# Kernel tuning notes

Hardware: AMD Instinct MI355X
Metric: run time of the kernel (lower is better)

The kernel has to match this reference:

```python
import jax, jax.numpy as jnp
import numpy as np

BN_EPS = 1e-5


def _bn(x, gamma, beta):
    # training-mode BatchNorm1d: biased batch stats over the edge/batch axis
    mean = jnp.mean(x, axis=0, keepdims=True)
    var = jnp.mean((x - mean) ** 2, axis=0, keepdims=True)
    return (x - mean) * jax.lax.rsqrt(var + BN_EPS) * gamma + beta


def setup_inputs() -> dict:
    key = jax.random.key(0)
    ks = jax.random.split(key, 20)
    N, E = 20000, 300000
    in_drug, in_prot, hidden = 256, 512, 256
    h2 = 2 * hidden

    def u(k, shape, fan_in):
        b = 1.0 / np.sqrt(fan_in)
        return jax.random.uniform(k, shape, jnp.float32, -b, b)

    return {
        "x_drug": jax.random.normal(ks[0], (N, in_drug), jnp.float32),
        "x_prot": jax.random.normal(ks[1], (N, in_prot), jnp.float32),
        "edge_index": jax.random.randint(ks[2], (2, E), 0, N, jnp.int64),
        "W_src": u(ks[3], (hidden, in_drug), in_drug),
        "W_dst": u(ks[4], (hidden, in_prot), in_prot),
        "W_gate": u(ks[5], (h2, h2), h2),
        "b_gate": u(ks[6], (h2,), h2),
        "W1": u(ks[7], (hidden, h2), h2),
        "b1": u(ks[8], (hidden,), h2),
        "g1": jnp.ones((hidden,), jnp.float32),
        "be1": jnp.zeros((hidden,), jnp.float32),
        "W2": u(ks[9], (hidden, hidden), hidden),
        "b2": u(ks[10], (hidden,), hidden),
        "g2": jnp.ones((hidden,), jnp.float32),
        "be2": jnp.zeros((hidden,), jnp.float32),
        "W3": u(ks[11], (1, hidden), hidden),
        "b3": u(ks[12], (1,), hidden),
        "W_bil": u(ks[13], (1, hidden, hidden), hidden),
        "b_bil": u(ks[14], (1,), hidden),
    }


def reference(x_drug, x_prot, edge_index, W_src, W_dst, W_gate, b_gate,
              W1, b1, g1, be1, W2, b2, g2, be2, W3, b3, W_bil, b_bil):
    src, dst = edge_index[0], edge_index[1]
    h_src = x_drug[src] @ W_src.T            # [E, H]
    h_dst = x_prot[dst] @ W_dst.T            # [E, H]
    h_cat = jnp.concatenate([h_src, h_dst], axis=1)  # [E, 2H]
    gate = jax.nn.sigmoid(h_cat @ W_gate.T + b_gate)
    h = gate * h_cat
    # MLP (dropout is identity here)
    h1 = jax.nn.relu(_bn(h @ W1.T + b1, g1, be1))
    h2_ = jax.nn.relu(_bn(h1 @ W2.T + b2, g2, be2))
    mlp_score = (h2_ @ W3.T + b3).reshape(-1)
    # Bilinear: out_ek = sum_ij h_src_ei W_kij h_dst_ej + b_k
    bil_score = (jnp.einsum("ei,kij,ej->ek", h_src, W_bil, h_dst) + b_bil).reshape(-1)
    return mlp_score + bil_score
```

## Files before the change

### kernel.cpp

```cpp
#include <hip/hip_runtime.h>
#include <hip/hip_bf16.h>

typedef unsigned short u16;
typedef __attribute__((ext_vector_type(8))) short bf16x8;
typedef __attribute__((ext_vector_type(8))) unsigned short us8;
typedef __attribute__((ext_vector_type(4))) float f32x4;


__device__ __forceinline__ float b2f(u16 u) {
    union { unsigned u32; float f; } x; x.u32 = ((unsigned)u) << 16; return x.f;
}
__device__ __forceinline__ u16 f2b(float f) {
    union { float f; unsigned u; } x; x.f = f;
    unsigned r = x.u + 0x7fffu + ((x.u >> 16) & 1u);
    return (u16)(r >> 16);
}

__global__ __launch_bounds__(256) void zero_kernel(float* p, int n) {
    int i = blockIdx.x * 256 + threadIdx.x;
    if (i < n) p[i] = 0.f;
}

struct CvtSeg { const float* in; u16* out; int n4; };
struct CvtArr { CvtSeg s[6]; int tot4; };
__global__ __launch_bounds__(256) void cvt_fused(CvtArr ca) {
    int i = blockIdx.x * 256 + threadIdx.x;
    if (i >= ca.tot4) return;
    int k = 0, off = i;
#pragma unroll
    for (int q = 0; q < 6; ++q) {
        if (off < ca.s[q].n4) { k = q; break; }
        off -= ca.s[q].n4;
    }
    float4 v = ((const float4*)ca.s[k].in)[off];
    ushort4 o; o.x = f2b(v.x); o.y = f2b(v.y); o.z = f2b(v.z); o.w = f2b(v.w);
    ((ushort4*)ca.s[k].out)[off] = o;
}

struct GDesc {
    const void* A; int lda; int a_f32;
    const u16* W; int ldb;
    u16* C; int ldc;
    int K;
    const float* bias;
};
template <int NY> struct GDescArr { GDesc d[NY]; };

template <int NY>
__global__ __launch_bounds__(256, 2) void mfma_node(GDescArr<NY> da, int M)
{
    const GDesc dd = da.d[blockIdx.y];
    __shared__ u16 As[2][128][40];
    __shared__ u16 Bs[2][256][40];
    const int t = threadIdx.x;
    const int row0 = blockIdx.x * 128;
    const int arow = t >> 1, aks = (t & 1) * 16;
    const int agr = min(row0 + arow, M - 1);
    const int w = t >> 6, lane = t & 63;
    const int wr = w >> 1, wc = w & 1;
    const int lrow = lane & 15, lkg = lane >> 4;
    const int NIT = dd.K >> 5;

    f32x4 acc[4][8] = {};
    us8 ar[2], br[4];
    float4 fr[4];

    auto load_regs = [&](int it) {
        const int k0 = it << 5;
        if (dd.a_f32) {
            const float* ap = (const float*)dd.A + (size_t)agr * dd.lda + k0 + aks;
#pragma unroll
            for (int q = 0; q < 4; ++q) fr[q] = *(const float4*)(ap + q * 4);
        } else {
            const u16* ap = (const u16*)dd.A + (size_t)agr * dd.lda + k0 + aks;
            ar[0] = *(const us8*)ap; ar[1] = *(const us8*)(ap + 8);
        }
        const u16* wp = dd.W + (size_t)t * dd.ldb + k0;
#pragma unroll
        for (int q = 0; q < 4; ++q) br[q] = *(const us8*)(wp + q * 8);
    };
    auto proc_write = [&](int b) {
        if (dd.a_f32) {
#pragma unroll
            for (int q = 0; q < 2; ++q) {
                us8 o;
                const float fq[8] = {fr[q*2].x, fr[q*2].y, fr[q*2].z, fr[q*2].w,
                                     fr[q*2+1].x, fr[q*2+1].y, fr[q*2+1].z, fr[q*2+1].w};
#pragma unroll
                for (int j = 0; j < 8; ++j) o[j] = f2b(fq[j]);
                *(us8*)&As[b][arow][aks + q * 8] = o;
            }
        } else {
            *(us8*)&As[b][arow][aks] = ar[0];
            *(us8*)&As[b][arow][aks + 8] = ar[1];
        }
#pragma unroll
        for (int q = 0; q < 4; ++q) *(us8*)&Bs[b][t][q * 8] = br[q];
    };
    auto do_mfma = [&](int b) {
        bf16x8 af[4];
#pragma unroll
        for (int mi = 0; mi < 4; ++mi)
            af[mi] = *(const bf16x8*)&As[b][wr * 64 + mi * 16 + lrow][lkg * 8];
#pragma unroll
        for (int ni = 0; ni < 8; ++ni) {
            bf16x8 bfr = *(const bf16x8*)&Bs[b][wc * 128 + ni * 16 + lrow][lkg * 8];
#pragma unroll
            for (int mi = 0; mi < 4; ++mi)
                acc[mi][ni] = __builtin_amdgcn_mfma_f32_16x16x32_bf16(
                    af[mi], bfr, acc[mi][ni], 0, 0, 0);
        }
    };

    load_regs(0); proc_write(0); __syncthreads();
    for (int it = 0; it < NIT; ++it) {
        const int cur = it & 1;
        if (it + 1 < NIT) load_regs(it + 1);
        do_mfma(cur);
        if (it + 1 < NIT) proc_write(cur ^ 1);
        __syncthreads();
    }

#pragma unroll
    for (int ni = 0; ni < 8; ++ni) {
        const int gcol = wc * 128 + ni * 16 + lrow;
        const float bv = dd.bias ? dd.bias[gcol] : 0.f;
#pragma unroll
        for (int mi = 0; mi < 4; ++mi) {
            f32x4 v = acc[mi][ni];
#pragma unroll
            for (int j = 0; j < 4; ++j) {
                const int grow = row0 + wr * 64 + mi * 16 + lkg * 4 + j;
                if (grow < M) dd.C[(size_t)grow * dd.ldc + gcol] = f2b(v[j] + bv);
            }
        }
    }
}

#define OP_GATE   1
#define OP_BNRELU 2

template <int AOP>
__global__ __launch_bounds__(256, 3) void mfma_edge(
    const u16* __restrict__ Ain,
    const u16* __restrict__ Wb, int ldb, int K,
    u16* __restrict__ C, int E,
    const int* __restrict__ ei,
    const u16* __restrict__ Gs, const u16* __restrict__ Gd,
    const u16* __restrict__ Hs, const u16* __restrict__ Hd,
    const u16* __restrict__ Bd, const float* __restrict__ b_bil,
    float* __restrict__ bil,
    const float* __restrict__ scaleK, const float* __restrict__ shiftK,
    float* __restrict__ sums)
{
    __shared__ u16 As[2][64][36];
    __shared__ float wsum[2][256];

    const int t = threadIdx.x;
    const int row0 = blockIdx.x * 64;
    const int arow = t >> 2;
    const int aks = (t & 3) * 8;
    const int agr = min(row0 + arow, E - 1);

    int s_ = 0, d_ = 0;
    if constexpr (AOP == OP_GATE) {
        s_ = ei[agr]; d_ = ei[E + agr];
    }

    const int lane = t & 63;
    const int wc = t >> 6;
    const int lrow = lane & 15, lkg = lane >> 4;
    const int NIT = K >> 5;

    f32x4 acc[4][4] = {};
    float bdot = 0.f;
    us8 g1r, g2r, hr, bdr;
    float4 sc0, sc1, sh0, sh1;

    auto load_regs = [&](int it) {
        const int k0 = it << 5;
        const int kg = k0 + aks;
        if constexpr (AOP == OP_GATE) {
            g1r = *(const us8*)(Gs + (size_t)s_ * 512 + kg);
            g2r = *(const us8*)(Gd + (size_t)d_ * 512 + kg);
            hr = (k0 < 256) ? *(const us8*)(Hs + (size_t)s_ * 256 + kg)
                            : *(const us8*)(Hd + (size_t)d_ * 256 + kg - 256);
            if (k0 < 256) bdr = *(const us8*)(Bd + (size_t)d_ * 256 + kg);
        } else {
            g1r = *(const us8*)(Ain + (size_t)agr * 256 + kg);
            sc0 = *(const float4*)(scaleK + kg);
            sc1 = *(const float4*)(scaleK + kg + 4);
            sh0 = *(const float4*)(shiftK + kg);
            sh1 = *(const float4*)(shiftK + kg + 4);
        }
    };
    auto proc_write = [&](int it, int b) {
        const int k0 = it << 5;
        us8 o;
        if constexpr (AOP == OP_GATE) {
#pragma unroll
            for (int j = 0; j < 8; ++j) {
                const float x = b2f(g1r[j]) + b2f(g2r[j]);
                const float g = 1.f / (1.f + __expf(-x));
                o[j] = f2b(g * b2f(hr[j]));
            }
            if (k0 < 256) {
#pragma unroll
                for (int j = 0; j < 8; ++j)
                    bdot = fmaf(b2f(hr[j]), b2f(bdr[j]), bdot);
            }
        } else {
            const float scq[8] = {sc0.x, sc0.y, sc0.z, sc0.w,
                                  sc1.x, sc1.y, sc1.z, sc1.w};
            const float shq[8] = {sh0.x, sh0.y, sh0.z, sh0.w,
                                  sh1.x, sh1.y, sh1.z, sh1.w};
#pragma unroll
            for (int j = 0; j < 8; ++j)
                o[j] = f2b(fmaxf(fmaf(b2f(g1r[j]), scq[j], shq[j]), 0.f));
        }
        *(us8*)&As[b][arow][aks] = o;
    };
    auto do_iter = [&](int it, int b) {
        const int k0 = it << 5;
        bf16x8 bfr[4];
#pragma unroll
        for (int ni = 0; ni < 4; ++ni)
            bfr[ni] = *(const bf16x8*)(Wb +
                (size_t)(wc * 64 + ni * 16 + lrow) * ldb + k0 + lkg * 8);
        bf16x8 af[4];
#pragma unroll
        for (int mi = 0; mi < 4; ++mi)
            af[mi] = *(const bf16x8*)&As[b][mi * 16 + lrow][lkg * 8];
#pragma unroll
        for (int ni = 0; ni < 4; ++ni)
#pragma unroll
            for (int mi = 0; mi < 4; ++mi)
                acc[mi][ni] = __builtin_amdgcn_mfma_f32_16x16x32_bf16(
                    af[mi], bfr[ni], acc[mi][ni], 0, 0, 0);
    };

    load_regs(0); proc_write(0, 0); __syncthreads();
    for (int it = 0; it < NIT; ++it) {
        const int cur = it & 1;
        if (it + 1 < NIT) load_regs(it + 1);
        do_iter(it, cur);
        if (it + 1 < NIT) proc_write(it + 1, cur ^ 1);
        __syncthreads();
    }

    if constexpr (AOP == OP_GATE) {
        bdot += __shfl_xor(bdot, 1, 64);
        bdot += __shfl_xor(bdot, 2, 64);
        if ((t & 3) == 0 && row0 + arow < E)
            bil[row0 + arow] = bdot + b_bil[0];
    }

#pragma unroll
    for (int ni = 0; ni < 4; ++ni) {
        const int gcol = wc * 64 + ni * 16 + lrow;
        float s = 0.f, ss = 0.f;
#pragma unroll
        for (int mi = 0; mi < 4; ++mi) {
            f32x4 v = acc[mi][ni];
#pragma unroll
            for (int j = 0; j < 4; ++j) {
                const int grow = row0 + mi * 16 + lkg * 4 + j;
                const float x = v[j];
                if (grow < E) {
                    C[(size_t)grow * 256 + gcol] = f2b(x);
                    s += x; ss = fmaf(x, x, ss);
                }
            }
        }
        s  += __shfl_xor(s, 16, 64);  s  += __shfl_xor(s, 32, 64);
        ss += __shfl_xor(ss, 16, 64); ss += __shfl_xor(ss, 32, 64);
        if (lkg == 0) { wsum[0][gcol] = s; wsum[1][gcol] = ss; }
    }
    __syncthreads();
    atomicAdd(&sums[t],       wsum[0][t]);
    atomicAdd(&sums[256 + t], wsum[1][t]);
}

__global__ void finalize_kernel(
    const float* __restrict__ sums, const float* __restrict__ g,
    const float* __restrict__ be, int M,
    float* __restrict__ scale, float* __restrict__ shift)
{
    const int c = threadIdx.x;
    const float inv = 1.f / (float)M;
    const float mean = sums[c] * inv;
    const float var  = sums[256 + c] * inv - mean * mean;
    const float sc = g[c] * rsqrtf(var + 1e-5f);
    scale[c] = sc;
    shift[c] = fmaf(-mean, sc, be[c]);
}

__global__ __launch_bounds__(256) void final_kernel(
    const u16* __restrict__ Z2,
    const float* __restrict__ scale2, const float* __restrict__ shift2,
    const float* __restrict__ W3, const float* __restrict__ b3,
    const float* __restrict__ bil,
    float* __restrict__ out, int E)
{
    const int w = threadIdx.x >> 6, lane = threadIdx.x & 63;
    const int e = blockIdx.x * 4 + w;
    if (e >= E) return;
    ushort4 zv = *(const ushort4*)(Z2 + (size_t)e * 256 + lane * 4);
    float4 sc = *(const float4*)(scale2 + lane * 4);
    float4 sh = *(const float4*)(shift2 + lane * 4);
    float4 w3 = *(const float4*)(W3 + lane * 4);
    const u16 zq[4] = {zv.x, zv.y, zv.z, zv.w};
    const float scq[4] = {sc.x, sc.y, sc.z, sc.w};
    const float shq[4] = {sh.x, sh.y, sh.z, sh.w};
    const float wq[4] = {w3.x, w3.y, w3.z, w3.w};
    float acc = 0.f;
#pragma unroll
    for (int i = 0; i < 4; ++i) {
        const float x = fmaxf(fmaf(b2f(zq[i]), scq[i], shq[i]), 0.f);
        acc = fmaf(x, wq[i], acc);
    }
#pragma unroll
    for (int off = 32; off; off >>= 1) acc += __shfl_down(acc, off, 64);
    if (lane == 0) out[e] = acc + b3[0] + bil[e];
}

extern "C" void kernel_launch(void* const* d_in, const int* in_sizes, int n_in,
                              void* d_out, int out_size, void* d_ws, size_t ws_size,
                              hipStream_t stream)
{
    const float* x_drug = (const float*)d_in[0];
    const float* x_prot = (const float*)d_in[1];
    const int*   ei     = (const int*)d_in[2];
    const float* W_src  = (const float*)d_in[3];
    const float* W_dst  = (const float*)d_in[4];
    const float* W_gate = (const float*)d_in[5];
    const float* b_gate = (const float*)d_in[6];
    const float* W1     = (const float*)d_in[7];
    const float* g1     = (const float*)d_in[9];
    const float* be1    = (const float*)d_in[10];
    const float* W2     = (const float*)d_in[11];
    const float* g2     = (const float*)d_in[13];
    const float* be2    = (const float*)d_in[14];
    const float* W3     = (const float*)d_in[15];
    const float* b3     = (const float*)d_in[16];
    const float* W_bil  = (const float*)d_in[17];
    const float* b_bil  = (const float*)d_in[18];
    float* out = (float*)d_out;

    const int N = in_sizes[0] / 256;
    const int E = in_sizes[2] / 2;

    char* wp_ = (char*)d_ws;
    auto alloc = [&](size_t bytes) {
        char* p = wp_; wp_ += (bytes + 255) & ~(size_t)255; return p;
    };
    u16* Wsrcb  = (u16*)alloc(256 * 256 * 2);
    u16* Wdstb  = (u16*)alloc(256 * 512 * 2);
    u16* Wgateb = (u16*)alloc(512 * 512 * 2);
    u16* Wbilb  = (u16*)alloc(256 * 256 * 2);
    u16* W1b    = (u16*)alloc(256 * 512 * 2);
    u16* W2b    = (u16*)alloc(256 * 256 * 2);
    u16* Hs     = (u16*)alloc((size_t)N * 256 * 2);
    u16* Hd     = (u16*)alloc((size_t)N * 256 * 2);
    u16* Gs     = (u16*)alloc((size_t)N * 512 * 2);
    u16* Gd     = (u16*)alloc((size_t)N * 512 * 2);
    u16* Bd     = (u16*)alloc((size_t)N * 256 * 2);
    u16* z      = (u16*)alloc((size_t)E * 256 * 2);
    float* bil  = (float*)alloc((size_t)E * 4);
    float* sums   = (float*)alloc(1024 * 4);
    float* scale1 = (float*)alloc(256 * 4);
    float* shift1 = (float*)alloc(256 * 4);
    float* scale2 = (float*)alloc(256 * 4);
    float* shift2 = (float*)alloc(256 * 4);

    zero_kernel<<<4, 256, 0, stream>>>(sums, 1024);

    CvtArr ca;
    ca.s[0] = {W_src,  Wsrcb,  256 * 256 / 4};
    ca.s[1] = {W_dst,  Wdstb,  256 * 512 / 4};
    ca.s[2] = {W_gate, Wgateb, 512 * 512 / 4};
    ca.s[3] = {W_bil,  Wbilb,  256 * 256 / 4};
    ca.s[4] = {W1,     W1b,    256 * 512 / 4};
    ca.s[5] = {W2,     W2b,    256 * 256 / 4};
    ca.tot4 = 0;
    for (int q = 0; q < 6; ++q) ca.tot4 += ca.s[q].n4;
    cvt_fused<<<(ca.tot4 + 255) / 256, 256, 0, stream>>>(ca);

    const int gxN = (N + 127) / 128;
    const int gxE = (E + 63) / 64;

    GDescArr<2> p1;
    p1.d[0] = {x_drug, 256, 1, Wsrcb, 256, Hs, 256, 256, nullptr};
    p1.d[1] = {x_prot, 512, 1, Wdstb, 512, Hd, 256, 512, nullptr};
    mfma_node<2><<<dim3(gxN, 2), 256, 0, stream>>>(p1, N);

    GDescArr<5> p2;
    p2.d[0] = {Hs, 256, 0, Wgateb,                 512, Gs,       512, 256, b_gate};
    p2.d[1] = {Hs, 256, 0, Wgateb + 256 * 512,     512, Gs + 256, 512, 256, b_gate + 256};
    p2.d[2] = {Hd, 256, 0, Wgateb + 256,           512, Gd,       512, 256, nullptr};
    p2.d[3] = {Hd, 256, 0, Wgateb + 256 * 512 + 256, 512, Gd + 256, 512, 256, nullptr};
    p2.d[4] = {Hd, 256, 0, Wbilb,                  256, Bd,       256, 256, nullptr};
    mfma_node<5><<<dim3(gxN, 5), 256, 0, stream>>>(p2, N);

    mfma_edge<OP_GATE><<<gxE, 256, 0, stream>>>(
        nullptr, W1b, 512, 512, z, E,
        ei, Gs, Gd, Hs, Hd, Bd, b_bil, bil, nullptr, nullptr, sums);
    finalize_kernel<<<1, 256, 0, stream>>>(sums, g1, be1, E, scale1, shift1);

    mfma_edge<OP_BNRELU><<<gxE, 256, 0, stream>>>(
        z, W2b, 256, 256, z, E,
        nullptr, nullptr, nullptr, nullptr, nullptr, nullptr, nullptr, nullptr,
        scale1, shift1, sums + 512);
    finalize_kernel<<<1, 256, 0, stream>>>(sums + 512, g2, be2, E, scale2, shift2);

    final_kernel<<<(E + 3) / 4, 256, 0, stream>>>(
        z, scale2, shift2, W3, b3, bil, out, E);
}
```

Baseline: 630.4 us.

## Stage weight tiles in LDS with 64-wide K slabs in edge MFMA kernel

The edge GEMM kernel now cooperatively loads the 256xK weight slab into shared memory (one row per thread) instead of having each wave read weight fragments straight from global memory, and widens the K step from 32 to 64 per slab. The A-operand preprocessing (gate sigmoid or BN+ReLU) is moved into the register prefetch, with a single LDS buffer plus two barriers per slab. The min-blocks launch bound of 3 is dropped. This cuts redundant global and L2 traffic for weights and halves loop iterations, at the cost of a much larger LDS footprint (about 46 KB), higher register pressure and possibly lower occupancy.

```diff
diff --git a/kernel.cpp b/kernel.cpp
--- a/kernel.cpp
+++ b/kernel.cpp
@@ -141,7 +141,7 @@
 #define OP_BNRELU 2
 
 template <int AOP>
-__global__ __launch_bounds__(256, 3) void mfma_edge(
+__global__ __launch_bounds__(256) void mfma_edge(
     const u16* __restrict__ Ain,
     const u16* __restrict__ Wb, int ldb, int K,
     u16* __restrict__ C, int E,
@@ -153,98 +153,112 @@
     const float* __restrict__ scaleK, const float* __restrict__ shiftK,
     float* __restrict__ sums)
 {
-    __shared__ u16 As[2][64][36];
+    __shared__ u16 As[64][72];
+    __shared__ u16 Bs[256][72];
     __shared__ float wsum[2][256];
 
     const int t = threadIdx.x;
     const int row0 = blockIdx.x * 64;
     const int arow = t >> 2;
-    const int aks = (t & 3) * 8;
+    const int aks  = (t & 3) * 16;
     const int agr = min(row0 + arow, E - 1);
 
     int s_ = 0, d_ = 0;
-    if constexpr (AOP == OP_GATE) {
-        s_ = ei[agr]; d_ = ei[E + agr];
-    }
+    if constexpr (AOP == OP_GATE) { s_ = ei[agr]; d_ = ei[E + agr]; }
 
     const int lane = t & 63;
     const int wc = t >> 6;
     const int lrow = lane & 15, lkg = lane >> 4;
-    const int NIT = K >> 5;
+    const int NKS = K >> 6;
 
     f32x4 acc[4][4] = {};
     float bdot = 0.f;
-    us8 g1r, g2r, hr, bdr;
-    float4 sc0, sc1, sh0, sh1;
-
-    auto load_regs = [&](int it) {
-        const int k0 = it << 5;
-        const int kg = k0 + aks;
+    us8 aw0, aw1, br[8];
+
+    auto loadA = [&](int ks) {
+        const int k = ks * 64 + aks;
         if constexpr (AOP == OP_GATE) {
-            g1r = *(const us8*)(Gs + (size_t)s_ * 512 + kg);
-            g2r = *(const us8*)(Gd + (size_t)d_ * 512 + kg);
-            hr = (k0 < 256) ? *(const us8*)(Hs + (size_t)s_ * 256 + kg)
-                            : *(const us8*)(Hd + (size_t)d_ * 256 + kg - 256);
-            if (k0 < 256) bdr = *(const us8*)(Bd + (size_t)d_ * 256 + kg);
+            us8 gs0 = *(const us8*)(Gs + (size_t)s_ * 512 + k);
+            us8 gs1 = *(const us8*)(Gs + (size_t)s_ * 512 + k + 8);
+            us8 gd0 = *(const us8*)(Gd + (size_t)d_ * 512 + k);
+            us8 gd1 = *(const us8*)(Gd + (size_t)d_ * 512 + k + 8);
+            const u16* hp = (ks < 4) ? (Hs + (size_t)s_ * 256 + k)
+                                     : (Hd + (size_t)d_ * 256 + k - 256);
+            us8 h0 = *(const us8*)hp, h1 = *(const us8*)(hp + 8);
+#pragma unroll
+            for (int j = 0; j < 8; ++j) {
+                const float x0 = b2f(gs0[j]) + b2f(gd0[j]);
+                const float x1 = b2f(gs1[j]) + b2f(gd1[j]);
+                aw0[j] = f2b(b2f(h0[j]) / (1.f + __expf(-x0)));
+                aw1[j] = f2b(b2f(h1[j]) / (1.f + __expf(-x1)));
+            }
+            if (ks < 4) {
+                us8 bd0 = *(const us8*)(Bd + (size_t)d_ * 256 + k);
+                us8 bd1 = *(const us8*)(Bd + (size_t)d_ * 256 + k + 8);
+#pragma unroll
+                for (int j = 0; j < 8; ++j) {
+                    bdot = fmaf(b2f(h0[j]), b2f(bd0[j]), bdot);
+                    bdot = fmaf(b2f(h1[j]), b2f(bd1[j]), bdot);
+                }
+            }
         } else {
-            g1r = *(const us8*)(Ain + (size_t)agr * 256 + kg);
-            sc0 = *(const float4*)(scaleK + kg);
-            sc1 = *(const float4*)(scaleK + kg + 4);
-            sh0 = *(const float4*)(shiftK + kg);
-            sh1 = *(const float4*)(shiftK + kg + 4);
-        }
-    };
-    auto proc_write = [&](int it, int b) {
-        const int k0 = it << 5;
-        us8 o;
-        if constexpr (AOP == OP_GATE) {
+            us8 a0 = *(const us8*)(Ain + (size_t)agr * 256 + k);
+            us8 a1 = *(const us8*)(Ain + (size_t)agr * 256 + k + 8);
+            float4 c0 = *(const float4*)(scaleK + k);
+            float4 c1 = *(const float4*)(scaleK + k + 4);
+            float4 c2 = *(const float4*)(scaleK + k + 8);
+            float4 c3 = *(const float4*)(scaleK + k + 12);
+            float4 h0 = *(const float4*)(shiftK + k);
+            float4 h1 = *(const float4*)(shiftK + k + 4);
+            float4 h2 = *(const float4*)(shiftK + k + 8);
+            float4 h3 = *(const float4*)(shiftK + k + 12);
+            const float scq[16] = {c0.x,c0.y,c0.z,c0.w, c1.x,c1.y,c1.z,c1.w,
+                                   c2.x,c2.y,c2.z,c2.w, c3.x,c3.y,c3.z,c3.w};
+            const float shq[16] = {h0.x,h0.y,h0.z,h0.w, h1.x,h1.y,h1.z,h1.w,
+                                   h2.x,h2.y,h2.z,h2.w, h3.x,h3.y,h3.z,h3.w};
 #pragma unroll
             for (int j = 0; j < 8; ++j) {
-                const float x = b2f(g1r[j]) + b2f(g2r[j]);
-                const float g = 1.f / (1.f + __expf(-x));
-                o[j] = f2b(g * b2f(hr[j]));
-            }
-            if (k0 < 256) {
-#pragma unroll
-                for (int j = 0; j < 8; ++j)
-                    bdot = fmaf(b2f(hr[j]), b2f(bdr[j]), bdot);
-            }
-        } else {
-            const float scq[8] = {sc0.x, sc0.y, sc0.z, sc0.w,
-                                  sc1.x, sc1.y, sc1.z, sc1.w};
-            const float shq[8] = {sh0.x, sh0.y, sh0.z, sh0.w,
-                                  sh1.x, sh1.y, sh1.z, sh1.w};
-#pragma unroll
-            for (int j = 0; j < 8; ++j)
-                o[j] = f2b(fmaxf(fmaf(b2f(g1r[j]), scq[j], shq[j]), 0.f));
-        }
-        *(us8*)&As[b][arow][aks] = o;
-    };
-    auto do_iter = [&](int it, int b) {
-        const int k0 = it << 5;
-        bf16x8 bfr[4];
-#pragma unroll
-        for (int ni = 0; ni < 4; ++ni)
-            bfr[ni] = *(const bf16x8*)(Wb +
-                (size_t)(wc * 64 + ni * 16 + lrow) * ldb + k0 + lkg * 8);
-        bf16x8 af[4];
-#pragma unroll
-        for (int mi = 0; mi < 4; ++mi)
-            af[mi] = *(const bf16x8*)&As[b][mi * 16 + lrow][lkg * 8];
-#pragma unroll
-        for (int ni = 0; ni < 4; ++ni)
+                aw0[j] = f2b(fmaxf(fmaf(b2f(a0[j]), scq[j],     shq[j]),     0.f));
+                aw1[j] = f2b(fmaxf(fmaf(b2f(a1[j]), scq[8 + j], shq[8 + j]), 0.f));
+            }
+        }
+    };
+    auto loadB = [&](int ks) {
+        const u16* wp = Wb + (size_t)t * ldb + ks * 64;
+#pragma unroll
+        for (int q = 0; q < 8; ++q) br[q] = *(const us8*)(wp + q * 8);
+    };
+    auto writeLDS = [&]() {
+        *(us8*)&As[arow][aks]     = aw0;
+        *(us8*)&As[arow][aks + 8] = aw1;
+#pragma unroll
+        for (int q = 0; q < 8; ++q) *(us8*)&Bs[t][q * 8] = br[q];
+    };
+    auto mfma_slab = [&]() {
+#pragma unroll
+        for (int kk = 0; kk < 64; kk += 32) {
+            bf16x8 af[4], bf[4];
 #pragma unroll
             for (int mi = 0; mi < 4; ++mi)
-                acc[mi][ni] = __builtin_amdgcn_mfma_f32_16x16x32_bf16(
-                    af[mi], bfr[ni], acc[mi][ni], 0, 0, 0);
-    };
-
-    load_regs(0); proc_write(0, 0); __syncthreads();
-    for (int it = 0; it < NIT; ++it) {
-        const int cur = it & 1;
-        if (it + 1 < NIT) load_regs(it + 1);
-        do_iter(it, cur);
-        if (it + 1 < NIT) proc_write(it + 1, cur ^ 1);
+                af[mi] = *(const bf16x8*)&As[mi * 16 + lrow][kk + lkg * 8];
+#pragma unroll
+            for (int ni = 0; ni < 4; ++ni)
+                bf[ni] = *(const bf16x8*)&Bs[wc * 64 + ni * 16 + lrow][kk + lkg * 8];
+#pragma unroll
+            for (int ni = 0; ni < 4; ++ni)
+#pragma unroll
+                for (int mi = 0; mi < 4; ++mi)
+                    acc[mi][ni] = __builtin_amdgcn_mfma_f32_16x16x32_bf16(
+                        af[mi], bf[ni], acc[mi][ni], 0, 0, 0);
+        }
+    };
+
+    loadA(0); loadB(0);
+    for (int ks = 0; ks < NKS; ++ks) {
+        writeLDS();
+        __syncthreads();
+        if (ks + 1 < NKS) { loadA(ks + 1); loadB(ks + 1); }
+        mfma_slab();
         __syncthreads();
     }
 
```

Measured after the change: 602.1 us. 4.5% less time.
